# Performance work log

Hardware: AMD Instinct MI355X
Metric: run time of the kernel (lower is better)

The kernel has to match this reference:

```python
import jax, jax.numpy as jnp
import numpy as np


def setup_inputs() -> dict:
    key = jax.random.key(0)
    k1, k2, k3, k4 = jax.random.split(key, 4)
    B, S, I, H = 128, 512, 512, 1024
    bound = 1.0 / np.sqrt(H)
    x = jax.random.normal(k1, (B, S, I), dtype=jnp.float32)
    W = jax.random.uniform(k2, (I, 4 * H), dtype=jnp.float32, minval=-bound, maxval=bound)
    U = jax.random.uniform(k3, (H, 4 * H), dtype=jnp.float32, minval=-bound, maxval=bound)
    bias = jax.random.uniform(k4, (4 * H,), dtype=jnp.float32, minval=-bound, maxval=bound)
    return {"x": x, "W": W, "U": U, "bias": bias}


def reference(x, W, U, bias):
    B, S, I = x.shape
    H = U.shape[0]
    # Precompute input projection for all timesteps in one big GEMM (same math).
    xW = jnp.einsum("bsi,ig->bsg", x, W) + bias  # (B, S, 4H)

    def step(carry, xw_t):
        h_t, c_t = carry
        gates = xw_t + h_t @ U  # (B, 4H)
        f_t = jax.nn.sigmoid(gates[:, :H])
        i_t = jax.nn.sigmoid(gates[:, H:2 * H])
        g_t = jnp.tanh(gates[:, 2 * H:3 * H])
        o_t = jax.nn.sigmoid(gates[:, 3 * H:])
        c_t = f_t * c_t + i_t * g_t
        h_t = o_t * jnp.tanh(c_t)
        return (h_t, c_t), h_t

    h0 = jnp.zeros((B, H), dtype=x.dtype)
    c0 = jnp.zeros((B, H), dtype=x.dtype)
    (_, _), hs = jax.lax.scan(step, (h0, c0), jnp.swapaxes(xW, 0, 1))  # hs: (S, B, H)
    return jnp.sum(hs, axis=0) / S
```

## Files before the change

### kernel.cpp

```cpp
#include <hip/hip_runtime.h>
#include <cmath>

#define Bsz 128
#define Ssz 512
#define Isz 512
#define Hsz 1024
#define G4  4096
#define Ktot 1536
#define NT  64
#define KT  4
#define KSL 384

typedef short s8v __attribute__((ext_vector_type(8)));
typedef unsigned short u16x8 __attribute__((ext_vector_type(8)));
typedef float f32x16 __attribute__((ext_vector_type(16)));
typedef float f32x4  __attribute__((ext_vector_type(4)));

__device__ __forceinline__ unsigned short f2bf(float f) {
    unsigned u = __float_as_uint(f);
    u += 0x7fffu + ((u >> 16) & 1u);
    return (unsigned short)(u >> 16);
}
__device__ __forceinline__ float bf2f(unsigned short h) {
    return __uint_as_float(((unsigned)h) << 16);
}
__device__ __forceinline__ float fsig(float v) { return 1.f / (1.f + __expf(-v)); }
__device__ __forceinline__ float ftanh(float v) { return 2.f / (1.f + __expf(-2.f * v)) - 1.f; }

__global__ __launch_bounds__(256) void conv_wu(const float* __restrict__ W,
                                               const float* __restrict__ U,
                                               unsigned short* __restrict__ WUthi,
                                               unsigned short* __restrict__ WUtlo) {
    __shared__ float tile[32][33];
    const int tx = threadIdx.x & 31, ty = threadIdx.x >> 5;
    const int nb = blockIdx.x * 32, kb = blockIdx.y * 32;
    #pragma unroll
    for (int r = 0; r < 4; ++r) {
        int k = kb + ty + r * 8;
        float v = (k < Isz) ? W[(size_t)k * G4 + nb + tx]
                            : U[(size_t)(k - Isz) * G4 + nb + tx];
        tile[ty + r * 8][tx] = v;
    }
    __syncthreads();
    #pragma unroll
    for (int r = 0; r < 4; ++r) {
        int nl = ty + r * 8;
        int n  = nb + nl;
        int pn = ((n & 1023) << 2) | (n >> 10);
        float v = tile[tx][nl];
        unsigned short h = f2bf(v);
        size_t dst = (size_t)pn * Ktot + kb + tx;
        WUthi[dst] = h;
        WUtlo[dst] = f2bf(v - bf2f(h));
    }
}

__global__ __launch_bounds__(256) void lstm_init(const float* __restrict__ x,
                                                 const float* __restrict__ bias,
                                                 float* __restrict__ c, float* __restrict__ hsum,
                                                 unsigned short* __restrict__ hhi0, unsigned short* __restrict__ hlo0,
                                                 unsigned short* __restrict__ xthi0, unsigned short* __restrict__ xtlo0,
                                                 float* __restrict__ biasP, unsigned* __restrict__ cnt) {
    int idx = blockIdx.x * 256 + threadIdx.x;
    c[idx] = 0.f; hsum[idx] = 0.f; hhi0[idx] = 0; hlo0[idx] = 0;
    if (idx < Bsz * Isz) {
        int b = idx >> 9, i = idx & 511;
        float xv = x[(size_t)b * Ssz * Isz + i];
        unsigned short h = f2bf(xv);
        xthi0[idx] = h;
        xtlo0[idx] = f2bf(xv - bf2f(h));
    }
    if (idx < G4)  biasP[idx] = bias[((idx & 3) << 10) | (idx >> 2)];
    if (idx < 2048) cnt[idx] = 0u;
}

#define PITCH 72
#define A_HI 0
#define A_LO (128 * PITCH)
#define B_HI (2 * 128 * PITCH)
#define B_LO (2 * 128 * PITCH + 64 * PITCH)
#define SMEM_ELEMS (2 * 128 * PITCH + 2 * 64 * PITCH)

__global__ __launch_bounds__(512) void lstm_step(
    const unsigned short* __restrict__ WUthi, const unsigned short* __restrict__ WUtlo,
    const unsigned short* __restrict__ xthi,  const unsigned short* __restrict__ xtlo,
    const unsigned short* __restrict__ hhi_in, const unsigned short* __restrict__ hlo_in,
    const float* __restrict__ biasP, const float* __restrict__ x, int t,
    float* __restrict__ c_st, float* __restrict__ hsum,
    unsigned short* __restrict__ hhi_o, unsigned short* __restrict__ hlo_o,
    unsigned short* __restrict__ xthi_o, unsigned short* __restrict__ xtlo_o,
    float* __restrict__ P, unsigned* __restrict__ cnt,
    float* __restrict__ out) {
    extern __shared__ unsigned short sm[];
    unsigned short* sAhi = sm + A_HI;
    unsigned short* sAlo = sm + A_LO;
    unsigned short* sBhi = sm + B_HI;
    unsigned short* sBlo = sm + B_LO;

    const int tid = threadIdx.x, lane = tid & 63, w = tid >> 6;
    const int bid = blockIdx.x;
    const int nt = bid & 63, kt = bid >> 6;

    const int m31  = lane & 31;
    const int koct = (lane >> 5) << 3;
    const int mq = w & 3, nh = w >> 2;
    const int rowA = (mq * 32 + m31) * PITCH + koct;
    const int rowB = (nh * 32 + m31) * PITCH + koct;

    const int arow = tid >> 3, aoct = tid & 7;
    const int awr0 = arow * PITCH + aoct * 8;
    const int awr1 = (arow + 64) * PITCH + aoct * 8;

    f32x16 acc;
    #pragma unroll
    for (int i = 0; i < 16; ++i) acc[i] = 0.f;

    u16x8 rAh0, rAl0, rAh1, rAl1, rBh, rBl;
#define LOADCHUNK(KC) { \
        const int kb_ = kt * KSL + (KC) * 64; \
        const int kg_ = kb_ + aoct * 8; \
        if (kb_ < Isz) { \
            const size_t o0 = (size_t)arow * Isz + kg_, o1 = (size_t)(arow + 64) * Isz + kg_; \
            rAh0 = *(const u16x8*)&xthi[o0]; rAl0 = *(const u16x8*)&xtlo[o0]; \
            rAh1 = *(const u16x8*)&xthi[o1]; rAl1 = *(const u16x8*)&xtlo[o1]; \
        } else { \
            const size_t o0 = (size_t)arow * Hsz + (kg_ - Isz), o1 = (size_t)(arow + 64) * Hsz + (kg_ - Isz); \
            rAh0 = *(const u16x8*)&hhi_in[o0]; rAl0 = *(const u16x8*)&hlo_in[o0]; \
            rAh1 = *(const u16x8*)&hhi_in[o1]; rAl1 = *(const u16x8*)&hlo_in[o1]; \
        } \
        const size_t ob_ = (size_t)(nt * 64 + arow) * Ktot + kg_; \
        rBh = *(const u16x8*)&WUthi[ob_]; rBl = *(const u16x8*)&WUtlo[ob_]; \
    }

    LOADCHUNK(0);
    #pragma unroll
    for (int kc = 0; kc < 6; ++kc) {
        __syncthreads();
        *(u16x8*)&sAhi[awr0] = rAh0;
        *(u16x8*)&sAlo[awr0] = rAl0;
        *(u16x8*)&sAhi[awr1] = rAh1;
        *(u16x8*)&sAlo[awr1] = rAl1;
        *(u16x8*)&sBhi[awr0] = rBh;
        *(u16x8*)&sBlo[awr0] = rBl;
        if (kc < 5) LOADCHUNK(kc + 1);
        __syncthreads();
        #pragma unroll
        for (int s = 0; s < 4; ++s) {
            const int o = s * 16;
            s8v ah = *(const s8v*)&sAhi[rowA + o];
            s8v al = *(const s8v*)&sAlo[rowA + o];
            s8v bh = *(const s8v*)&sBhi[rowB + o];
            s8v bl = *(const s8v*)&sBlo[rowB + o];
            acc = __builtin_amdgcn_mfma_f32_32x32x16_bf16(ah, bh, acc, 0, 0, 0);
            acc = __builtin_amdgcn_mfma_f32_32x32x16_bf16(al, bh, acc, 0, 0, 0);
            acc = __builtin_amdgcn_mfma_f32_32x32x16_bf16(ah, bl, acc, 0, 0, 0);
        }
    }
#undef LOADCHUNK

    {
        float* Ps = P + (size_t)(kt * NT + nt) * (Bsz * 64);
        const int mb = mq * 32 + 4 * (lane >> 5);
        const int c0 = nh * 32 + m31;
        #pragma unroll
        for (int r = 0; r < 16; ++r) {
            int m = mb + (r & 3) + 8 * (r >> 2);
            float* p0 = Ps + m * 64 + c0;
            float v0 = acc[r];
            asm volatile("global_store_dword %0, %1, off sc0 sc1" :: "v"(p0), "v"(v0) : "memory");
        }
    }

    if (t + 1 < Ssz && tid < 256) {
        int idx = bid * 256 + tid;
        int bb = idx >> 9, ii = idx & 511;
        float xv = x[((size_t)bb * Ssz + (t + 1)) * Isz + ii];
        unsigned short xh = f2bf(xv);
        xthi_o[idx] = xh;
        xtlo_o[idx] = f2bf(xv - bf2f(xh));
    }

    __syncthreads();

    if (tid == 0) {
        unsigned* cp = &cnt[nt * 32];
        unsigned one = 1u;
        asm volatile("s_waitcnt vmcnt(0) lgkmcnt(0)" ::: "memory");
        asm volatile("global_atomic_add %0, %1, off sc1" :: "v"(cp), "v"(one) : "memory");
        const unsigned target = (unsigned)(KT * (t + 1));
        unsigned v;
        do {
            __builtin_amdgcn_s_sleep(1);
            asm volatile("global_load_dword %0, %1, off sc0 sc1\n\ts_waitcnt vmcnt(0)"
                         : "=v"(v) : "v"(cp) : "memory");
        } while (v < target);
    }
    __syncthreads();

    {
        const int jl = tid & 15;
        const int brow = kt * 32 + (tid >> 4);
        const int j = nt * 16 + jl;
        const float* Pb = P + ((size_t)nt * Bsz + brow) * 64 + jl * 4;
        const size_t kstride = (size_t)NT * Bsz * 64;
        f32x4 p0, p1, p2, p3;
        asm volatile("global_load_dwordx4 %0, %1, off sc0 sc1" : "=v"(p0) : "v"(Pb));
        asm volatile("global_load_dwordx4 %0, %1, off sc0 sc1" : "=v"(p1) : "v"(Pb + kstride));
        asm volatile("global_load_dwordx4 %0, %1, off sc0 sc1" : "=v"(p2) : "v"(Pb + 2 * kstride));
        asm volatile("global_load_dwordx4 %0, %1, off sc0 sc1" : "=v"(p3) : "v"(Pb + 3 * kstride));
        asm volatile("s_waitcnt vmcnt(0)" ::: "memory");
        __builtin_amdgcn_sched_barrier(0);
        f32x4 bp = *(const f32x4*)&biasP[(size_t)j * 4];
        float gf = bp.x + p0[0] + p1[0] + p2[0] + p3[0];
        float gi = bp.y + p0[1] + p1[1] + p2[1] + p3[1];
        float gg = bp.z + p0[2] + p1[2] + p2[2] + p3[2];
        float go = bp.w + p0[3] + p1[3] + p2[3] + p3[3];
        float f  = fsig(gf);
        float i_ = fsig(gi);
        float g  = ftanh(gg);
        float o  = fsig(go);
        size_t sidx = (size_t)brow * Hsz + j;
        float cn = f * c_st[sidx] + i_ * g;
        c_st[sidx] = cn;
        float hn = o * ftanh(cn);
        float hs = hsum[sidx] + hn;
        hsum[sidx] = hs;
        unsigned short hh = f2bf(hn);
        hhi_o[sidx] = hh;
        hlo_o[sidx] = f2bf(hn - bf2f(hh));
        if (t == Ssz - 1) out[sidx] = hs * (1.f / (float)Ssz);
    }
}

extern "C" void kernel_launch(void* const* d_in, const int* in_sizes, int n_in,
                              void* d_out, int out_size, void* d_ws, size_t ws_size,
                              hipStream_t stream) {
    const float* x    = (const float*)d_in[0];
    const float* W    = (const float*)d_in[1];
    const float* U    = (const float*)d_in[2];
    const float* bias = (const float*)d_in[3];
    float* out = (float*)d_out;

    unsigned char* base = (unsigned char*)d_ws;
    unsigned short* WUthi = (unsigned short*)(base);
    unsigned short* WUtlo = (unsigned short*)(base + 12582912);
    float*          P     = (float*)(base + 25165824);
    float*          c_st  = (float*)(base + 33554432);
    float*          hsum  = (float*)(base + 34078720);
    unsigned short* hh0   = (unsigned short*)(base + 34603008);
    unsigned short* hl0   = (unsigned short*)(base + 34865152);
    unsigned short* hh1   = (unsigned short*)(base + 35127296);
    unsigned short* hl1   = (unsigned short*)(base + 35389440);
    unsigned short* xh0   = (unsigned short*)(base + 35651584);
    unsigned short* xl0   = (unsigned short*)(base + 35782656);
    unsigned short* xh1   = (unsigned short*)(base + 35913728);
    unsigned short* xl1   = (unsigned short*)(base + 36044800);
    float*          biasP = (float*)(base + 36175872);
    unsigned*       cnt   = (unsigned*)(base + 36192256);

    unsigned short* xh[2] = {xh0, xh1};
    unsigned short* xl[2] = {xl0, xl1};
    unsigned short* hh[2] = {hh0, hh1};
    unsigned short* hl[2] = {hl0, hl1};

    conv_wu<<<dim3(G4 / 32, Ktot / 32), 256, 0, stream>>>(W, U, WUthi, WUtlo);
    lstm_init<<<(Bsz * Hsz) / 256, 256, 0, stream>>>(x, bias, c_st, hsum,
                                                     hh0, hl0, xh0, xl0, biasP, cnt);

    for (int t = 0; t < Ssz; ++t) {
        lstm_step<<<NT * KT, 512, SMEM_ELEMS * 2, stream>>>(
            WUthi, WUtlo, xh[t & 1], xl[t & 1], hh[t & 1], hl[t & 1],
            biasP, x, t, c_st, hsum,
            hh[(t + 1) & 1], hl[(t + 1) & 1], xh[(t + 1) & 1], xl[(t + 1) & 1],
            P, cnt, out);
    }
}
```

Measured before the change: 6.465 ms.

## Keep own K-slice partial in LDS and relax cache scope on partial-sum exchange

Each block's partial sum for the batch rows it finalizes now stays in shared memory instead of going through global memory. Only the other three K-slice partials are stored and reloaded from global. The global stores, loads and the spin-wait poll drop the sc0 bit and keep only sc1, which relaxes the cache coherence scope. This cuts one quarter of the cross-block traffic and per-access cache cost in each timestep. It also adds an extra barrier and depends on the relaxed scope still making the data visible across CUs.

```diff
diff --git a/kernel.cpp b/kernel.cpp
--- a/kernel.cpp
+++ b/kernel.cpp
@@ -70,7 +70,7 @@
         xthi0[idx] = h;
         xtlo0[idx] = f2bf(xv - bf2f(h));
     }
-    if (idx < G4)  biasP[idx] = bias[((idx & 3) << 10) | (idx >> 2)];
+    if (idx < G4)   biasP[idx] = bias[((idx & 3) << 10) | (idx >> 2)];
     if (idx < 2048) cnt[idx] = 0u;
 }
 
@@ -80,6 +80,10 @@
 #define B_HI (2 * 128 * PITCH)
 #define B_LO (2 * 128 * PITCH + 64 * PITCH)
 #define SMEM_ELEMS (2 * 128 * PITCH + 2 * 64 * PITCH)
+#define LREDP 68
+
+#define GLOAD16_DEV(dst, ptr) \
+    asm volatile("global_load_dwordx4 %0, %1, off sc1" : "=v"(dst) : "v"(ptr))
 
 __global__ __launch_bounds__(512) void lstm_step(
     const unsigned short* __restrict__ WUthi, const unsigned short* __restrict__ WUtlo,
@@ -158,18 +162,29 @@
     }
 #undef LOADCHUNK
 
+    __syncthreads();
+    float* Lred = (float*)sm;
     {
-        float* Ps = P + (size_t)(kt * NT + nt) * (Bsz * 64);
         const int mb = mq * 32 + 4 * (lane >> 5);
         const int c0 = nh * 32 + m31;
-        #pragma unroll
-        for (int r = 0; r < 16; ++r) {
-            int m = mb + (r & 3) + 8 * (r >> 2);
-            float* p0 = Ps + m * 64 + c0;
-            float v0 = acc[r];
-            asm volatile("global_store_dword %0, %1, off sc0 sc1" :: "v"(p0), "v"(v0) : "memory");
+        if (mq == kt) {
+            #pragma unroll
+            for (int r = 0; r < 16; ++r) {
+                int ml = 4 * (lane >> 5) + (r & 3) + 8 * (r >> 2);
+                Lred[ml * LREDP + c0] = acc[r];
+            }
+        } else {
+            float* Ps = P + (size_t)(kt * NT + nt) * (Bsz * 64);
+            #pragma unroll
+            for (int r = 0; r < 16; ++r) {
+                int m = mb + (r & 3) + 8 * (r >> 2);
+                float* p0 = Ps + m * 64 + c0;
+                float v0 = acc[r];
+                asm volatile("global_store_dword %0, %1, off sc1" :: "v"(p0), "v"(v0) : "memory");
+            }
         }
     }
+    asm volatile("s_waitcnt vmcnt(0)" ::: "memory");
 
     if (t + 1 < Ssz && tid < 256) {
         int idx = bid * 256 + tid;
@@ -191,7 +206,7 @@
         unsigned v;
         do {
             __builtin_amdgcn_s_sleep(1);
-            asm volatile("global_load_dword %0, %1, off sc0 sc1\n\ts_waitcnt vmcnt(0)"
+            asm volatile("global_load_dword %0, %1, off sc1\n\ts_waitcnt vmcnt(0)"
                          : "=v"(v) : "v"(cp) : "memory");
         } while (v < target);
     }
@@ -203,18 +218,21 @@
         const int j = nt * 16 + jl;
         const float* Pb = P + ((size_t)nt * Bsz + brow) * 64 + jl * 4;
         const size_t kstride = (size_t)NT * Bsz * 64;
-        f32x4 p0, p1, p2, p3;
-        asm volatile("global_load_dwordx4 %0, %1, off sc0 sc1" : "=v"(p0) : "v"(Pb));
-        asm volatile("global_load_dwordx4 %0, %1, off sc0 sc1" : "=v"(p1) : "v"(Pb + kstride));
-        asm volatile("global_load_dwordx4 %0, %1, off sc0 sc1" : "=v"(p2) : "v"(Pb + 2 * kstride));
-        asm volatile("global_load_dwordx4 %0, %1, off sc0 sc1" : "=v"(p3) : "v"(Pb + 3 * kstride));
+        const int sA_ = (kt == 0) ? 1 : 0;
+        const int sB_ = (kt <= 1) ? 2 : 1;
+        const int sC_ = (kt <= 2) ? 3 : 2;
+        f32x4 pA, pB, pC;
+        GLOAD16_DEV(pA, Pb + (size_t)sA_ * kstride);
+        GLOAD16_DEV(pB, Pb + (size_t)sB_ * kstride);
+        GLOAD16_DEV(pC, Pb + (size_t)sC_ * kstride);
+        f32x4 own = *(const f32x4*)&Lred[(tid >> 4) * LREDP + jl * 4];
         asm volatile("s_waitcnt vmcnt(0)" ::: "memory");
         __builtin_amdgcn_sched_barrier(0);
         f32x4 bp = *(const f32x4*)&biasP[(size_t)j * 4];
-        float gf = bp.x + p0[0] + p1[0] + p2[0] + p3[0];
-        float gi = bp.y + p0[1] + p1[1] + p2[1] + p3[1];
-        float gg = bp.z + p0[2] + p1[2] + p2[2] + p3[2];
-        float go = bp.w + p0[3] + p1[3] + p2[3] + p3[3];
+        float gf = bp.x + own[0] + pA[0] + pB[0] + pC[0];
+        float gi = bp.y + own[1] + pA[1] + pB[1] + pC[1];
+        float gg = bp.z + own[2] + pA[2] + pB[2] + pC[2];
+        float go = bp.w + own[3] + pA[3] + pB[3] + pC[3];
         float f  = fsig(gf);
         float i_ = fsig(gi);
         float g  = ftanh(gg);
```

New measurement: 6.631 ms. 1.03x slower.
